# Optimization experiments

Measured on AMD Instinct MI355X. Metric: run time of the kernel, lower is better.

Reference implementation:

```python
import jax, jax.numpy as jnp
import numpy as np

HEADS = 4
DIM_HEAD = 128
DIM = 128
INNER = HEADS * DIM_HEAD  # 512
MAX_POS = 100
SCALE = DIM_HEAD ** -0.5


def setup_inputs() -> dict:
    key = jax.random.key(0)
    ks = jax.random.split(key, 8)
    b, h, w = 2, 48, 64
    fmap1 = jax.random.normal(ks[0], (b, DIM, h, w), jnp.float32)
    fmap2 = jax.random.normal(ks[1], (b, DIM, h, w), jnp.float32)
    Wqk = jax.random.normal(ks[2], (2 * INNER, DIM), jnp.float32) * 0.05
    Wv = jax.random.normal(ks[3], (INNER, DIM), jnp.float32) * 0.05
    rel_h = jax.random.normal(ks[4], (2 * MAX_POS - 1, DIM_HEAD), jnp.float32) * 0.05
    rel_w = jax.random.normal(ks[5], (2 * MAX_POS - 1, DIM_HEAD), jnp.float32) * 0.05
    Wp = jax.random.normal(ks[6], (DIM, INNER), jnp.float32) * 0.05
    gamma = jnp.full((1,), 0.1, jnp.float32)  # nonzero so the attn path is active
    return {"fmap1": fmap1, "fmap2": fmap2, "Wqk": Wqk, "Wv": Wv,
            "rel_h": rel_h, "rel_w": rel_w, "Wp": Wp, "gamma": gamma}


def _aggregate(fmap, Wqk, Wv, rel_h, rel_w, Wp, gamma):
    b, c, H, W = fmap.shape
    # 1x1 conv = channel matmul
    qk = jnp.einsum('oc,bchw->bohw', Wqk, fmap)
    q = qk[:, :INNER] * SCALE  # k chunk unused (position-only similarity)
    # b (n d) h w -> b n h w d
    q = q.reshape(b, HEADS, DIM_HEAD, H, W).transpose(0, 1, 3, 4, 2)
    v = jnp.einsum('oc,bchw->bohw', Wv, fmap)
    v = v.reshape(b, HEADS, DIM_HEAD, H, W).transpose(0, 1, 3, 4, 2).reshape(b, HEADS, H * W, DIM_HEAD)
    # relative position similarity (RelPosEmb)
    idx_h = jnp.arange(H)[:, None] - jnp.arange(H)[None, :] + (MAX_POS - 1)  # (H,H)
    idx_w = jnp.arange(W)[:, None] - jnp.arange(W)[None, :] + (MAX_POS - 1)  # (W,W)
    He = rel_h[idx_h]  # (x,u,d)
    We = rel_w[idx_w]  # (y,v,d)
    hs = jnp.einsum('bnxyd,xud->bnxyu', q, He)  # (b,n,x,y,u)
    ws = jnp.einsum('bnxyd,yvd->bnxyv', q, We)  # (b,n,x,y,v)
    sim = hs[..., :, None] + ws[..., None, :]   # (b,n,x,y,u,v)
    sim = sim.reshape(b, HEADS, H * W, H * W)
    attn = jax.nn.softmax(sim, axis=-1)
    out = jnp.einsum('bnij,bnjd->bnid', attn, v)  # (b,n,hw,d)
    out = out.reshape(b, HEADS, H, W, DIM_HEAD).transpose(0, 1, 4, 2, 3).reshape(b, INNER, H, W)
    out = jnp.einsum('oc,bchw->bohw', Wp, out)  # project (dim != inner_dim)
    return fmap + gamma[0] * out


def reference(fmap1, fmap2, Wqk, Wv, rel_h, rel_w, Wp, gamma):
    out1 = _aggregate(fmap1, Wqk, Wv, rel_h, rel_w, Wp, gamma)
    out2 = _aggregate(fmap2, Wqk, Wv, rel_h, rel_w, Wp, gamma)
    return (out1, out2)
```

## Files before the change

### kernel.cpp

```cpp
#include <hip/hip_runtime.h>
#include <cstdint>
#include <cstddef>

typedef short bf16x8 __attribute__((ext_vector_type(8)));
typedef float f32x4 __attribute__((ext_vector_type(4)));

#define HH 48
#define WW 64
#define HWSZ 3072
#define SCALE_Q 0.08838834764831845f

__device__ __forceinline__ float b2f(unsigned short u) {
    union { unsigned int i; float f; } c; c.i = ((unsigned int)u) << 16; return c.f;
}
__device__ __forceinline__ unsigned short f2b(float f) {
    union { float f; unsigned int i; } c; c.f = f;
    unsigned int r = (c.i + 0x7fffu + ((c.i >> 16) & 1u)) >> 16;
    return (unsigned short)r;
}

__global__ __launch_bounds__(256) void k_prep(const float* __restrict__ f0,
                                              const float* __restrict__ f1,
                                              const float* __restrict__ Wqk,
                                              const float* __restrict__ Wv,
                                              const float* __restrict__ Wp,
                                              unsigned short* __restrict__ Xb,
                                              unsigned short* __restrict__ Wcat,
                                              unsigned short* __restrict__ Wpb) {
    int bid = blockIdx.x;
    int tid = threadIdx.x;
    if (bid < 1536) {
        __shared__ float t[32][33];
        int px = bid % 96, rest = bid / 96;
        int cy = rest & 3, fb = rest >> 2;
        int f = fb >> 1, bb = fb & 1;
        const float* src = f ? f1 : f0;
        int pT = px * 32, cT = cy * 32;
        int tx = tid & 31, ty = tid >> 5;
#pragma unroll
        for (int i = 0; i < 4; ++i) {
            int c = cT + ty + i * 8, pos = pT + tx;
            t[ty + i * 8][tx] = src[(size_t)(bb * 128 + c) * HWSZ + pos];
        }
        __syncthreads();
#pragma unroll
        for (int i = 0; i < 4; ++i) {
            int pos = pT + ty + i * 8, c = cT + tx;
            Xb[(size_t)(fb * HWSZ + pos) * 128 + c] = f2b(t[tx][ty + i * 8]);
        }
    } else {
        int idx = (bid - 1536) * 256 + tid;
        if (idx < 131072) {
            int o = idx >> 7, c = idx & 127;
            float v = (o < 512) ? Wqk[o * 128 + c] * SCALE_Q : Wv[(o - 512) * 128 + c];
            Wcat[idx] = f2b(v);
        } else {
            int j = idx - 131072;
            Wpb[j] = f2b(Wp[j]);
        }
    }
}

__global__ __launch_bounds__(256) void k_qv(const unsigned short* __restrict__ Xb,
                                            const unsigned short* __restrict__ Wcat,
                                            unsigned short* __restrict__ Qx,
                                            unsigned short* __restrict__ Vt) {
    __shared__ unsigned short Asub[64 * 136];
    __shared__ unsigned short Bsub[128 * 136];
    int mt = blockIdx.x, nt = blockIdx.y, fb = blockIdx.z;
    int tid = threadIdx.x;
    const unsigned short* asrc = Xb + (size_t)(fb * HWSZ + mt * 64) * 128;
    const unsigned short* bsrc = Wcat + (size_t)nt * 128 * 128;
    for (int ch = tid; ch < 1024; ch += 256) {
        int row = ch >> 4, seg = ch & 15;
        *(bf16x8*)&Asub[row * 136 + seg * 8] = *(const bf16x8*)(asrc + ch * 8);
    }
    for (int ch = tid; ch < 2048; ch += 256) {
        int row = ch >> 4, seg = ch & 15;
        *(bf16x8*)&Bsub[row * 136 + seg * 8] = *(const bf16x8*)(bsrc + ch * 8);
    }
    __syncthreads();
    int l = tid & 63, w = tid >> 6;
    int wm = w >> 1, wn = w & 1;
    int lr = l & 15, lk8 = (l >> 4) * 8;
    f32x4 acc[2][4] = {};
#pragma unroll
    for (int kt = 0; kt < 4; ++kt) {
        bf16x8 a[2], b[4];
#pragma unroll
        for (int m = 0; m < 2; ++m)
            a[m] = *(const bf16x8*)&Asub[(wm * 32 + m * 16 + lr) * 136 + kt * 32 + lk8];
#pragma unroll
        for (int n = 0; n < 4; ++n)
            b[n] = *(const bf16x8*)&Bsub[(wn * 64 + n * 16 + lr) * 136 + kt * 32 + lk8];
#pragma unroll
        for (int m = 0; m < 2; ++m)
#pragma unroll
            for (int n = 0; n < 4; ++n)
                acc[m][n] = __builtin_amdgcn_mfma_f32_16x16x32_bf16(a[m], b[n], acc[m][n], 0, 0, 0);
    }
    int f = fb >> 1, bb = fb & 1;
#pragma unroll
    for (int m = 0; m < 2; ++m)
#pragma unroll
        for (int n = 0; n < 4; ++n) {
            int o = nt * 128 + wn * 64 + n * 16 + lr;
            int pos0 = mt * 64 + wm * 32 + m * 16 + (l >> 4) * 4;
            if (o < 512) {
                int nh = o >> 7, d = o & 127;
#pragma unroll
                for (int r = 0; r < 4; ++r) {
                    int pos = pos0 + r, x = pos >> 6, y = pos & 63;
                    Qx[(size_t)((f * 48 + x) * 512 + (bb * 4 + nh) * 64 + y) * 128 + d] = f2b(acc[m][n][r]);
                }
            } else {
                int oo = o - 512, nh = oo >> 7, d = oo & 127;
                uint2 val;
                val.x = (unsigned int)f2b(acc[m][n][0]) | ((unsigned int)f2b(acc[m][n][1]) << 16);
                val.y = (unsigned int)f2b(acc[m][n][2]) | ((unsigned int)f2b(acc[m][n][3]) << 16);
                *(uint2*)&Vt[(size_t)((fb * 4 + nh) * 128 + d) * HWSZ + pos0] = val;
            }
        }
}

__global__ __launch_bounds__(256) void k_sm(const unsigned short* __restrict__ Qx,
                                            const float* __restrict__ rel_h,
                                            const float* __restrict__ rel_w,
                                            unsigned short* __restrict__ PH,
                                            unsigned short* __restrict__ PW) {
    __shared__ float sm[4][16][68];
    int bid = blockIdx.x;
    int tid = threadIdx.x, l = tid & 63, w = tid >> 6;
    int lr = l & 15, lk8 = (l >> 4) * 8;
    if (bid < 384) {
        int x = bid % 48, f = (bid / 48) & 1, mtz = bid / 96;
        bf16x8 bh[3][4];
#pragma unroll
        for (int ut = 0; ut < 3; ++ut) {
            int u = ut * 16 + lr, rr = x - u + 99;
#pragma unroll
            for (int kt = 0; kt < 4; ++kt) {
                const float* s = rel_h + rr * 128 + kt * 32 + lk8;
                float4 a0 = *(const float4*)s, a1 = *(const float4*)(s + 4);
                bf16x8 pk;
                pk[0] = (short)f2b(a0.x); pk[1] = (short)f2b(a0.y); pk[2] = (short)f2b(a0.z); pk[3] = (short)f2b(a0.w);
                pk[4] = (short)f2b(a1.x); pk[5] = (short)f2b(a1.y); pk[6] = (short)f2b(a1.z); pk[7] = (short)f2b(a1.w);
                bh[ut][kt] = pk;
            }
        }
        const unsigned short* qbase = Qx + (size_t)(f * 48 + x) * 512 * 128;
        unsigned short* phbase = PH + (size_t)(f * 48 + x) * 512 * 48;
        for (int mt = mtz * 2; mt < mtz * 2 + 2; ++mt) {
            int rg = w * 128 + mt * 16 + lr;
            const unsigned short* qrow = qbase + (size_t)rg * 128;
            bf16x8 a[4];
#pragma unroll
            for (int kt = 0; kt < 4; ++kt) a[kt] = *(const bf16x8*)(qrow + kt * 32 + lk8);
            f32x4 acc[3] = {};
#pragma unroll
            for (int kt = 0; kt < 4; ++kt)
#pragma unroll
                for (int ut = 0; ut < 3; ++ut)
                    acc[ut] = __builtin_amdgcn_mfma_f32_16x16x32_bf16(a[kt], bh[ut][kt], acc[ut], 0, 0, 0);
            __syncthreads();
#pragma unroll
            for (int ut = 0; ut < 3; ++ut)
#pragma unroll
                for (int r = 0; r < 4; ++r)
                    sm[w][(l >> 4) * 4 + r][ut * 16 + lr] = acc[ut][r];
            __syncthreads();
            int part = l >> 4;
            float vb[12];
            float mx = -1e30f;
#pragma unroll
            for (int j = 0; j < 12; ++j) { vb[j] = sm[w][lr][part * 12 + j]; mx = fmaxf(mx, vb[j]); }
            mx = fmaxf(mx, __shfl_xor(mx, 16, 64));
            mx = fmaxf(mx, __shfl_xor(mx, 32, 64));
            float ssum = 0.f;
#pragma unroll
            for (int j = 0; j < 12; ++j) { vb[j] = __expf(vb[j] - mx); ssum += vb[j]; }
            ssum += __shfl_xor(ssum, 16, 64);
            ssum += __shfl_xor(ssum, 32, 64);
            float inv = 1.0f / ssum;
            unsigned short* dst = phbase + (size_t)(w * 128 + mt * 16 + lr) * 48 + part * 12;
#pragma unroll
            for (int j = 0; j < 12; ++j) dst[j] = f2b(vb[j] * inv);
        }
    } else {
        int b2 = bid - 384;
        int y = b2 % 64, f = (b2 / 64) & 1, mtz = b2 / 128;
        bf16x8 bw[4][4];
#pragma unroll
        for (int vt = 0; vt < 4; ++vt) {
            int v = vt * 16 + lr, rr = y - v + 99;
#pragma unroll
            for (int kt = 0; kt < 4; ++kt) {
                const float* s = rel_w + rr * 128 + kt * 32 + lk8;
                float4 a0 = *(const float4*)s, a1 = *(const float4*)(s + 4);
                bf16x8 pk;
                pk[0] = (short)f2b(a0.x); pk[1] = (short)f2b(a0.y); pk[2] = (short)f2b(a0.z); pk[3] = (short)f2b(a0.w);
                pk[4] = (short)f2b(a1.x); pk[5] = (short)f2b(a1.y); pk[6] = (short)f2b(a1.z); pk[7] = (short)f2b(a1.w);
                bw[vt][kt] = pk;
            }
        }
        for (int mt = mtz * 2; mt < mtz * 2 + 2; ++mt) {
            int rg = w * 96 + mt * 16 + lr;
            int bn = rg / 48, xx = rg - bn * 48;
            const unsigned short* qrow = Qx + (size_t)((f * 48 + xx) * 512 + bn * 64 + y) * 128;
            bf16x8 a[4];
#pragma unroll
            for (int kt = 0; kt < 4; ++kt) a[kt] = *(const bf16x8*)(qrow + kt * 32 + lk8);
            f32x4 acc[4] = {};
#pragma unroll
            for (int kt = 0; kt < 4; ++kt)
#pragma unroll
                for (int vt = 0; vt < 4; ++vt)
                    acc[vt] = __builtin_amdgcn_mfma_f32_16x16x32_bf16(a[kt], bw[vt][kt], acc[vt], 0, 0, 0);
            __syncthreads();
#pragma unroll
            for (int vt = 0; vt < 4; ++vt)
#pragma unroll
                for (int r = 0; r < 4; ++r)
                    sm[w][(l >> 4) * 4 + r][vt * 16 + lr] = acc[vt][r];
            __syncthreads();
            int part = l >> 4;
            float vb[16];
            float mx = -1e30f;
#pragma unroll
            for (int j = 0; j < 16; ++j) { vb[j] = sm[w][lr][part * 16 + j]; mx = fmaxf(mx, vb[j]); }
            mx = fmaxf(mx, __shfl_xor(mx, 16, 64));
            mx = fmaxf(mx, __shfl_xor(mx, 32, 64));
            float ssum = 0.f;
#pragma unroll
            for (int j = 0; j < 16; ++j) { vb[j] = __expf(vb[j] - mx); ssum += vb[j]; }
            ssum += __shfl_xor(ssum, 16, 64);
            ssum += __shfl_xor(ssum, 32, 64);
            float inv = 1.0f / ssum;
            unsigned short* dst = PW + (size_t)((f * 64 + y) * 384 + rg) * 64 + part * 16;
#pragma unroll
            for (int j = 0; j < 16; ++j) dst[j] = f2b(vb[j] * inv);
        }
    }
}

__global__ __launch_bounds__(256, 3) void k_attn(const unsigned short* __restrict__ PH,
                                                 const unsigned short* __restrict__ PW,
                                                 const unsigned short* __restrict__ Vt,
                                                 unsigned short* __restrict__ AO) {
    __shared__ unsigned short phl[48 * 128];
    __shared__ unsigned short vbuf[2][64 * 64];
    int bid = blockIdx.x;
    int r16 = bid & 15;
    int rest = bid >> 4;
    int t = rest >> 1, dh = rest & 1;
    int fbn = (r16 & 7) * 2 + (r16 >> 3);
    int f = fbn >> 3, bidx = (fbn >> 2) & 1, nh = fbn & 3;
    int fb = f * 2 + bidx, bn = bidx * 4 + nh;
    int tid = threadIdx.x;
    int l = tid & 63, wd = tid >> 6;
    int lr = l & 15, lg = l >> 4, lk8 = lg * 8;

    const unsigned short* vsrc = Vt + (size_t)((fb * 4 + nh) * 128 + dh * 64) * HWSZ;
    int sd = tid >> 3, sch = tid & 7;
    const unsigned short* vsrow0 = vsrc + (size_t)sd * HWSZ + sch * 8;
    const unsigned short* vsrow1 = vsrc + (size_t)(sd + 32) * HWSZ + sch * 8;
    int wo0 = sd * 64 + ((sch ^ (sd & 7)) * 8);
    int wo1 = (sd + 32) * 64 + ((sch ^ (sd & 7)) * 8);

    bf16x8 r0a = *(const bf16x8*)(vsrow0);
    bf16x8 r0b = *(const bf16x8*)(vsrow1);

    for (int i = tid; i < 3072; i += 256) {
        int up2 = i >> 7, q = i & 127;
        int xy = t * 128 + q, x = xy >> 6, y = xy & 63;
        unsigned int wv = *(const unsigned int*)(PH + ((size_t)(f * 48 + x) * 512 + bn * 64 + y) * 48 + up2 * 2);
        int qoff = (q & 15) * 8 + (q >> 4);
        phl[(up2 * 2) * 128 + qoff]     = (unsigned short)(wv & 0xffffu);
        phl[(up2 * 2 + 1) * 128 + qoff] = (unsigned short)(wv >> 16);
    }
    bf16x8 b[8][2];
#pragma unroll
    for (int n = 0; n < 8; ++n) {
        int xy = t * 128 + n * 16 + lr;
        int x = xy >> 6, y = xy & 63;
        const unsigned short* pwr = PW + ((size_t)(f * 64 + y) * 384 + bn * 48 + x) * 64;
        b[n][0] = *(const bf16x8*)(pwr + lk8);
        b[n][1] = *(const bf16x8*)(pwr + 32 + lk8);
    }
    *(bf16x8*)&vbuf[0][wo0] = r0a;
    *(bf16x8*)&vbuf[0][wo1] = r0b;
    __syncthreads();

    int arow = wd * 16 + lr;
    int ao0 = arow * 64 + ((lg ^ (arow & 7)) * 8);
    int ao1 = arow * 64 + (((4 + lg) ^ (arow & 7)) * 8);
    const unsigned short* phrow = &phl[lr * 8];
    f32x4 acc[8] = {};
    const f32x4 zero4 = {0.f, 0.f, 0.f, 0.f};
    int cur = 0;
    for (int u = 0; u < 48; ++u) {
        bf16x8 ra, rb;
        if (u < 47) {
            ra = *(const bf16x8*)(vsrow0 + (size_t)(u + 1) * 64);
            rb = *(const bf16x8*)(vsrow1 + (size_t)(u + 1) * 64);
        }
        bf16x8 av0 = *(const bf16x8*)&vbuf[cur][ao0];
        bf16x8 av1 = *(const bf16x8*)&vbuf[cur][ao1];
        bf16x8 phv = *(const bf16x8*)(phrow + u * 128);
#pragma unroll
        for (int n = 0; n < 8; ++n) {
            f32x4 Y = __builtin_amdgcn_mfma_f32_16x16x32_bf16(av0, b[n][0], zero4, 0, 0, 0);
            Y = __builtin_amdgcn_mfma_f32_16x16x32_bf16(av1, b[n][1], Y, 0, 0, 0);
            float p = b2f((unsigned short)phv[n]);
            acc[n] += p * Y;
        }
        if (u < 47) {
            *(bf16x8*)&vbuf[cur ^ 1][wo0] = ra;
            *(bf16x8*)&vbuf[cur ^ 1][wo1] = rb;
        }
        __syncthreads();
        cur ^= 1;
    }
    unsigned short* aobase = AO + (size_t)fb * HWSZ * 512 + nh * 128 + dh * 64 + wd * 16 + lg * 4;
#pragma unroll
    for (int n = 0; n < 8; ++n) {
        int q = t * 128 + n * 16 + lr;
        uint2 val;
        val.x = (unsigned int)f2b(acc[n][0]) | ((unsigned int)f2b(acc[n][1]) << 16);
        val.y = (unsigned int)f2b(acc[n][2]) | ((unsigned int)f2b(acc[n][3]) << 16);
        *(uint2*)(aobase + (size_t)q * 512) = val;
    }
}

__global__ __launch_bounds__(256) void k_proj(const unsigned short* __restrict__ AO,
                                              const unsigned short* __restrict__ Wpb,
                                              const float* __restrict__ f0,
                                              const float* __restrict__ f1,
                                              const float* __restrict__ gamma,
                                              float* __restrict__ out) {
    __shared__ unsigned short Asub[32 * 136];
    __shared__ unsigned short Bsub[128 * 136];
    int t = blockIdx.x, fb = blockIdx.y;
    int f = fb >> 1, bb = fb & 1;
    int tid = threadIdx.x;
    int l = tid & 63, w = tid >> 6;
    int wm = w >> 1, wn = w & 1;
    int lr = l & 15, lk8 = (l >> 4) * 8;
    f32x4 acc[4] = {};
    for (int ks = 0; ks < 4; ++ks) {
        if (ks) __syncthreads();
        for (int ch = tid; ch < 512; ch += 256) {
            int row = ch >> 4, seg = ch & 15;
            *(bf16x8*)&Asub[row * 136 + seg * 8] =
                *(const bf16x8*)(AO + (size_t)(fb * HWSZ + t * 32 + row) * 512 + ks * 128 + seg * 8);
        }
        for (int ch = tid; ch < 2048; ch += 256) {
            int row = ch >> 4, seg = ch & 15;
            *(bf16x8*)&Bsub[row * 136 + seg * 8] =
                *(const bf16x8*)(Wpb + (size_t)row * 512 + ks * 128 + seg * 8);
        }
        __syncthreads();
#pragma unroll
        for (int kt = 0; kt < 4; ++kt) {
            bf16x8 a, b[4];
            a = *(const bf16x8*)&Asub[(wm * 16 + lr) * 136 + kt * 32 + lk8];
#pragma unroll
            for (int n = 0; n < 4; ++n)
                b[n] = *(const bf16x8*)&Bsub[(wn * 64 + n * 16 + lr) * 136 + kt * 32 + lk8];
#pragma unroll
            for (int n = 0; n < 4; ++n)
                acc[n] = __builtin_amdgcn_mfma_f32_16x16x32_bf16(a, b[n], acc[n], 0, 0, 0);
        }
    }
    const float* fmapf = f ? f1 : f0;
    float g = gamma[0];
#pragma unroll
    for (int n = 0; n < 4; ++n) {
        int c = wn * 64 + n * 16 + lr;
        int pos0 = t * 32 + wm * 16 + (l >> 4) * 4;
        size_t addr = (size_t)(bb * 128 + c) * HWSZ + pos0;
        float4 fv = *(const float4*)(fmapf + addr);
        float4 ov;
        ov.x = fv.x + g * acc[n][0];
        ov.y = fv.y + g * acc[n][1];
        ov.z = fv.z + g * acc[n][2];
        ov.w = fv.w + g * acc[n][3];
        *(float4*)(out + (size_t)f * 786432 + addr) = ov;
    }
}

extern "C" void kernel_launch(void* const* d_in, const int* in_sizes, int n_in,
                              void* d_out, int out_size, void* d_ws, size_t ws_size,
                              hipStream_t stream) {
    (void)in_sizes; (void)n_in; (void)out_size; (void)ws_size;
    const float* fmap1 = (const float*)d_in[0];
    const float* fmap2 = (const float*)d_in[1];
    const float* Wqk   = (const float*)d_in[2];
    const float* Wv    = (const float*)d_in[3];
    const float* rel_h = (const float*)d_in[4];
    const float* rel_w = (const float*)d_in[5];
    const float* Wp    = (const float*)d_in[6];
    const float* gamma = (const float*)d_in[7];
    float* out = (float*)d_out;
    char* ws = (char*)d_ws;

    unsigned short* Xb   = (unsigned short*)(ws + 0);
    unsigned short* Wcat = (unsigned short*)(ws + 3145728);
    unsigned short* Wpb  = (unsigned short*)(ws + 3407872);
    unsigned short* Qx   = (unsigned short*)(ws + 3538944);
    unsigned short* AO   = Qx;
    unsigned short* Vt   = (unsigned short*)(ws + 16121856);
    unsigned short* PH   = (unsigned short*)(ws + 28704768);
    unsigned short* PW   = (unsigned short*)(ws + 33423360);

    k_prep<<<dim3(2304), dim3(256), 0, stream>>>(fmap1, fmap2, Wqk, Wv, Wp, Xb, Wcat, Wpb);
    k_qv<<<dim3(48, 8, 4), dim3(256), 0, stream>>>(Xb, Wcat, Qx, Vt);
    k_sm<<<dim3(768), dim3(256), 0, stream>>>(Qx, rel_h, rel_w, PH, PW);
    k_attn<<<dim3(768), dim3(256), 0, stream>>>(PH, PW, Vt, AO);
    k_proj<<<dim3(96, 4), dim3(256), 0, stream>>>(AO, Wpb, fmap1, fmap2, gamma, out);
}
```

Baseline: 103.1 us.

## Store V as per-row [u][d][v] tiles and load MFMA operands directly from global

The V projection output is re-laid out as (head, row u, d, column v) so each attention-loop iteration reads a contiguous d-by-64 tile. k_attn drops the double-buffered LDS staging of V and its per-iteration __syncthreads. Each wave now loads its MFMA A operands straight from global memory with a one-iteration register prefetch. This removes LDS traffic and barriers, but each wave issues its own global loads, which puts more pressure on cache and latency hiding.

Measured after the change: 105.3 us. +2.1%, slower.

```diff
diff --git a/kernel.cpp b/kernel.cpp
--- a/kernel.cpp
+++ b/kernel.cpp
@@ -115,10 +115,11 @@
                 }
             } else {
                 int oo = o - 512, nh = oo >> 7, d = oo & 127;
+                int u = pos0 >> 6, v = pos0 & 63;
                 uint2 val;
                 val.x = (unsigned int)f2b(acc[m][n][0]) | ((unsigned int)f2b(acc[m][n][1]) << 16);
                 val.y = (unsigned int)f2b(acc[m][n][2]) | ((unsigned int)f2b(acc[m][n][3]) << 16);
-                *(uint2*)&Vt[(size_t)((fb * 4 + nh) * 128 + d) * HWSZ + pos0] = val;
+                *(uint2*)&Vt[(((size_t)(fb * 4 + nh) * 48 + u) * 128 + d) * 64 + v] = val;
             }
         }
 }
@@ -248,7 +249,6 @@
                                                  const unsigned short* __restrict__ Vt,
                                                  unsigned short* __restrict__ AO) {
     __shared__ unsigned short phl[48 * 128];
-    __shared__ unsigned short vbuf[2][64 * 64];
     int bid = blockIdx.x;
     int r16 = bid & 15;
     int rest = bid >> 4;
@@ -260,16 +260,6 @@
     int l = tid & 63, wd = tid >> 6;
     int lr = l & 15, lg = l >> 4, lk8 = lg * 8;
 
-    const unsigned short* vsrc = Vt + (size_t)((fb * 4 + nh) * 128 + dh * 64) * HWSZ;
-    int sd = tid >> 3, sch = tid & 7;
-    const unsigned short* vsrow0 = vsrc + (size_t)sd * HWSZ + sch * 8;
-    const unsigned short* vsrow1 = vsrc + (size_t)(sd + 32) * HWSZ + sch * 8;
-    int wo0 = sd * 64 + ((sch ^ (sd & 7)) * 8);
-    int wo1 = (sd + 32) * 64 + ((sch ^ (sd & 7)) * 8);
-
-    bf16x8 r0a = *(const bf16x8*)(vsrow0);
-    bf16x8 r0b = *(const bf16x8*)(vsrow1);
-
     for (int i = tid; i < 3072; i += 256) {
         int up2 = i >> 7, q = i & 127;
         int xy = t * 128 + q, x = xy >> 6, y = xy & 63;
@@ -287,39 +277,29 @@
         b[n][0] = *(const bf16x8*)(pwr + lk8);
         b[n][1] = *(const bf16x8*)(pwr + 32 + lk8);
     }
-    *(bf16x8*)&vbuf[0][wo0] = r0a;
-    *(bf16x8*)&vbuf[0][wo1] = r0b;
+    const unsigned short* vrow = Vt + (size_t)(fb * 4 + nh) * 48 * 8192
+                                    + (size_t)(dh * 64 + wd * 16 + lr) * 64 + lk8;
+    bf16x8 A0 = *(const bf16x8*)(vrow);
+    bf16x8 A1 = *(const bf16x8*)(vrow + 32);
     __syncthreads();
 
-    int arow = wd * 16 + lr;
-    int ao0 = arow * 64 + ((lg ^ (arow & 7)) * 8);
-    int ao1 = arow * 64 + (((4 + lg) ^ (arow & 7)) * 8);
     const unsigned short* phrow = &phl[lr * 8];
     f32x4 acc[8] = {};
     const f32x4 zero4 = {0.f, 0.f, 0.f, 0.f};
-    int cur = 0;
     for (int u = 0; u < 48; ++u) {
-        bf16x8 ra, rb;
+        bf16x8 N0 = A0, N1 = A1;
         if (u < 47) {
-            ra = *(const bf16x8*)(vsrow0 + (size_t)(u + 1) * 64);
-            rb = *(const bf16x8*)(vsrow1 + (size_t)(u + 1) * 64);
-        }
-        bf16x8 av0 = *(const bf16x8*)&vbuf[cur][ao0];
-        bf16x8 av1 = *(const bf16x8*)&vbuf[cur][ao1];
+            N0 = *(const bf16x8*)(vrow + (size_t)(u + 1) * 8192);
+            N1 = *(const bf16x8*)(vrow + (size_t)(u + 1) * 8192 + 32);
+        }
         bf16x8 phv = *(const bf16x8*)(phrow + u * 128);
 #pragma unroll
         for (int n = 0; n < 8; ++n) {
-            f32x4 Y = __builtin_amdgcn_mfma_f32_16x16x32_bf16(av0, b[n][0], zero4, 0, 0, 0);
-            Y = __builtin_amdgcn_mfma_f32_16x16x32_bf16(av1, b[n][1], Y, 0, 0, 0);
-            float p = b2f((unsigned short)phv[n]);
-            acc[n] += p * Y;
-        }
-        if (u < 47) {
-            *(bf16x8*)&vbuf[cur ^ 1][wo0] = ra;
-            *(bf16x8*)&vbuf[cur ^ 1][wo1] = rb;
-        }
-        __syncthreads();
-        cur ^= 1;
+            f32x4 Y = __builtin_amdgcn_mfma_f32_16x16x32_bf16(A0, b[n][0], zero4, 0, 0, 0);
+            Y = __builtin_amdgcn_mfma_f32_16x16x32_bf16(A1, b[n][1], Y, 0, 0, 0);
+            acc[n] += b2f((unsigned short)phv[n]) * Y;
+        }
+        A0 = N0; A1 = N1;
     }
     unsigned short* aobase = AO + (size_t)fb * HWSZ * 512 + nh * 128 + dh * 64 + wd * 16 + lg * 4;
 #pragma unroll
```
